# Optimization experiments

Hardware: AMD Instinct MI355X
Metric: run time of the kernel (lower is better)

The kernel has to match this reference:

```python
import jax, jax.numpy as jnp
import numpy as np

ALPHA = 1.702
LIMIT = 7.0
EPS = 1e-5
TOP_K = 4


def setup_inputs() -> dict:
    key = jax.random.key(0)
    ks = jax.random.split(key, 8)
    B, S, H, I, E = 2, 512, 2048, 2048, 16
    return {
        "x": jax.random.normal(ks[0], (B, S, H), jnp.float32),
        "norm_w": jnp.ones((H,), jnp.float32),
        "gate_w": jax.random.normal(ks[1], (E, H), jnp.float32) * 0.02,
        "gate_b": jax.random.normal(ks[2], (E,), jnp.float32) * 0.02,
        "w1": jax.random.normal(ks[3], (E, 2 * I, H), jnp.float32) * 0.02,
        "b1": jax.random.normal(ks[4], (E, 2 * I), jnp.float32) * 0.02,
        "w2": jax.random.normal(ks[5], (E, H, I), jnp.float32) * 0.02,
        "b2": jax.random.normal(ks[6], (E, H), jnp.float32) * 0.02,
    }


def reference(x, norm_w, gate_w, gate_b, w1, b1, w2, b2):
    B, S, H = x.shape
    M = B * S
    E = gate_w.shape[0]
    xf = x.reshape(M, H)
    # RMSNorm
    t = xf * jax.lax.rsqrt(jnp.mean(xf * xf, axis=-1, keepdims=True) + EPS) * norm_w
    # Router: top-k over logits, then softmax over the selected k (sm_first=False)
    logits = t @ gate_w.T + gate_b  # [M, E]
    vals, idx = jax.lax.top_k(logits, TOP_K)
    gates_k = jax.nn.softmax(vals, axis=-1)  # [M, k]
    # Scatter top-k gate weights into dense [M, E] combine matrix
    G = jnp.zeros((M, E), x.dtype).at[jnp.arange(M)[:, None], idx].set(gates_k)
    # Expert MLP1 (all experts, combined sparsely below): [E, M, 2I]
    h = jnp.einsum('mh,eoh->emo', t, w1) + b1[:, None, :]
    # SwiGLU with clamp (gpt-oss): interleaved gate/linear columns
    a = jnp.minimum(h[..., ::2], LIMIT)
    b = jnp.clip(h[..., 1::2], -LIMIT, LIMIT)
    act = a * jax.nn.sigmoid(ALPHA * a) * (b + 1.0)  # [E, M, I]
    # Expert MLP2: [E, M, H]
    y = jnp.einsum('emi,edi->emd', act, w2) + b2[:, None, :]
    # Combine with gate weights (gammas scale full per-expert output incl. bias)
    delta = jnp.einsum('me,emd->md', G, y)
    return x + delta.reshape(B, S, H)
```

## Files before the change

kernel.cpp:

```cpp
#include <hip/hip_runtime.h>
#include <hip/hip_bf16.h>

constexpr int MTOK = 1024;
constexpr int HDIM = 2048;
constexpr int IDIM = 2048;
constexpr int NEXP = 16;
constexpr int TOPK = 4;
constexpr int NA   = MTOK * TOPK;

#define ALPHA_C 1.702f
#define LIMIT_C 7.0f
#define RMS_EPS 1e-5f

using short8 = __attribute__((ext_vector_type(8))) short;
using f32x4  = __attribute__((ext_vector_type(4))) float;

__device__ __forceinline__ unsigned short f2bf(float f) {
    unsigned u = __builtin_bit_cast(unsigned, f);
    u += 0x7fffu + ((u >> 16) & 1u);
    return (unsigned short)(u >> 16);
}

__device__ __forceinline__ unsigned pack2bf(float lo, float hi) {
    return (unsigned)f2bf(lo) | ((unsigned)f2bf(hi) << 16);
}

__device__ __forceinline__ short8 cvt8(const float4 a, const float4 b) {
    union { short8 s; unsigned u[4]; } r;
    r.u[0] = pack2bf(a.x, a.y);
    r.u[1] = pack2bf(a.z, a.w);
    r.u[2] = pack2bf(b.x, b.y);
    r.u[3] = pack2bf(b.z, b.w);
    return r.s;
}

__global__ __launch_bounds__(256) void k_router(
    const float* __restrict__ x, const float* __restrict__ norm_w,
    const float* __restrict__ gate_w, const float* __restrict__ gate_b,
    float* __restrict__ out,
    unsigned short* __restrict__ t_bf,
    int* __restrict__ counts, int* __restrict__ idx_of,
    int* __restrict__ slot_of, float* __restrict__ gate_mk)
{
    __shared__ float t_lds[HDIM];
    __shared__ float red[4];
    __shared__ float logits[NEXP];

    const int m   = blockIdx.x;
    const int tid = threadIdx.x;
    const float* xr = x + (size_t)m * HDIM;

    float4 v0 = ((const float4*)xr)[tid * 2];
    float4 v1 = ((const float4*)xr)[tid * 2 + 1];
    ((float4*)(out + (size_t)m * HDIM))[tid * 2]     = v0;
    ((float4*)(out + (size_t)m * HDIM))[tid * 2 + 1] = v1;

    float ss = v0.x*v0.x + v0.y*v0.y + v0.z*v0.z + v0.w*v0.w
             + v1.x*v1.x + v1.y*v1.y + v1.z*v1.z + v1.w*v1.w;
    #pragma unroll
    for (int off = 32; off > 0; off >>= 1) ss += __shfl_down(ss, off);
    if ((tid & 63) == 0) red[tid >> 6] = ss;
    __syncthreads();
    float tot = red[0] + red[1] + red[2] + red[3];
    float scale = rsqrtf(tot / (float)HDIM + RMS_EPS);

    float4 n0 = ((const float4*)norm_w)[tid * 2];
    float4 n1 = ((const float4*)norm_w)[tid * 2 + 1];
    float t[8];
    t[0]=v0.x*scale*n0.x; t[1]=v0.y*scale*n0.y; t[2]=v0.z*scale*n0.z; t[3]=v0.w*scale*n0.w;
    t[4]=v1.x*scale*n1.x; t[5]=v1.y*scale*n1.y; t[6]=v1.z*scale*n1.z; t[7]=v1.w*scale*n1.w;
    short8 pk;
    #pragma unroll
    for (int j = 0; j < 8; ++j) {
        t_lds[tid * 8 + j] = t[j];
        pk[j] = (short)f2bf(t[j]);
    }
    *(short8*)(t_bf + (size_t)m * HDIM + tid * 8) = pk;
    __syncthreads();

    const int e = tid >> 4, j = tid & 15;
    const float4* gw4 = (const float4*)(gate_w + (size_t)e * HDIM);
    const float4* tl4 = (const float4*)t_lds;
    float part = 0.f;
    for (int h4 = j; h4 < HDIM / 4; h4 += 16) {
        float4 g = gw4[h4], tv = tl4[h4];
        part += g.x*tv.x + g.y*tv.y + g.z*tv.z + g.w*tv.w;
    }
    #pragma unroll
    for (int off = 8; off > 0; off >>= 1) part += __shfl_xor(part, off);
    if (j == 0) logits[e] = part + gate_b[e];
    __syncthreads();

    if (tid == 0) {
        float lv[NEXP];
        #pragma unroll
        for (int q = 0; q < NEXP; ++q) lv[q] = logits[q];
        int   sel[TOPK];
        float sv[TOPK];
        #pragma unroll
        for (int k = 0; k < TOPK; ++k) {
            float best = -1e30f; int bi = 0;
            for (int q = 0; q < NEXP; ++q)
                if (lv[q] > best) { best = lv[q]; bi = q; }
            sel[k] = bi; sv[k] = best; lv[bi] = -1e30f;
        }
        float mx = sv[0], s = 0.f, g[TOPK];
        #pragma unroll
        for (int k = 0; k < TOPK; ++k) { g[k] = __expf(sv[k] - mx); s += g[k]; }
        float inv = 1.f / s;
        #pragma unroll
        for (int k = 0; k < TOPK; ++k) {
            int a = m * TOPK + k;
            int slot = atomicAdd(&counts[sel[k]], 1);
            idx_of[a]  = sel[k];
            slot_of[a] = slot;
            gate_mk[a] = g[k] * inv;
        }
    }
}

__global__ void k_remap(const int* __restrict__ idx_of, const int* __restrict__ slot_of,
                        const float* __restrict__ gate_mk, const int* __restrict__ counts,
                        int* __restrict__ token_of, float* __restrict__ gate_row)
{
    int a = blockIdx.x * blockDim.x + threadIdx.x;
    if (a >= NA) return;
    int e = idx_of[a];
    int off = 0;
    for (int q = 0; q < NEXP; ++q) off += (q < e) ? counts[q] : 0;
    int r = off + slot_of[a];
    token_of[r] = a >> 2;
    gate_row[r] = gate_mk[a];
}

__global__ __launch_bounds__(256) void k_gemm1(
    const unsigned short* __restrict__ t_bf,
    const float* __restrict__ w1, const float* __restrict__ b1,
    const int* __restrict__ counts, const int* __restrict__ token_of,
    unsigned short* __restrict__ act)
{
    __shared__ unsigned char lB[2][5120];

    const int e = blockIdx.z;
    int ne = 0, roff = 0;
    #pragma unroll
    for (int q = 0; q < NEXP; ++q) {
        int cq = counts[q];
        roff += (q < e) ? cq : 0;
        ne    = (q == e) ? cq : ne;
    }
    const int brow = blockIdx.y * 320;
    if (brow >= ne) return;
    const int i0 = blockIdx.x * 32;
    const int tid = threadIdx.x;

    const int wv = tid >> 6, ln = tid & 63;
    const int lr = ln & 15, lk = ln >> 4;
    const int br = tid >> 2, bp = tid & 3;

    const unsigned short* aptr[5];
    #pragma unroll
    for (int mf = 0; mf < 5; ++mf) {
        int rg = brow + wv * 80 + mf * 16 + lr;
        int tok = token_of[roff + (rg < ne ? rg : 0)];
        aptr[mf] = t_bf + (size_t)tok * HDIM + lk * 8;
    }
    const int o = (br < 32) ? (2 * (i0 + br)) : (2 * (i0 + br - 32) + 1);
    const float* bsrc = w1 + ((size_t)e * (2 * IDIM) + o) * HDIM + bp * 8;

    short8 aS[2][5];
    float4 bS[4][2];
    f32x4  acc[5][4] = {};

    {
        float4 p0 = *(const float4*)(bsrc);
        float4 p1 = *(const float4*)(bsrc + 4);
        *(short8*)(&lB[0][br * 80 + bp * 16]) = cvt8(p0, p1);
    }
    bS[1][0] = *(const float4*)(bsrc + 32);  bS[1][1] = *(const float4*)(bsrc + 36);
    bS[2][0] = *(const float4*)(bsrc + 64);  bS[2][1] = *(const float4*)(bsrc + 68);
    bS[3][0] = *(const float4*)(bsrc + 96);  bS[3][1] = *(const float4*)(bsrc + 100);
    #pragma unroll
    for (int mf = 0; mf < 5; ++mf) {
        aS[0][mf] = *(const short8*)(aptr[mf]);
        aS[1][mf] = *(const short8*)(aptr[mf] + 32);
    }
    asm volatile("s_waitcnt lgkmcnt(0)" ::: "memory");
    __builtin_amdgcn_s_barrier();

#define GSTEP(T, P)                                                                          \
    {                                                                                        \
        const int t_ = (T);                                                                  \
        if (t_ + 1 < 64)                                                                     \
            *(short8*)(&lB[((P) & 1) ^ 1][br * 80 + bp * 16]) =                              \
                cvt8(bS[((P) + 1) & 3][0], bS[((P) + 1) & 3][1]);                            \
        if (t_ + 4 < 64) {                                                                   \
            bS[(P)][0] = *(const float4*)(bsrc + (t_ + 4) * 32);                             \
            bS[(P)][1] = *(const float4*)(bsrc + (t_ + 4) * 32 + 4);                         \
        }                                                                                    \
        short8 bfr[4];                                                                       \
        _Pragma("unroll")                                                                    \
        for (int n = 0; n < 4; ++n)                                                          \
            bfr[n] = *(const short8*)(&lB[(P) & 1][(n * 16 + lr) * 80 + lk * 16]);           \
        _Pragma("unroll")                                                                    \
        for (int mf = 0; mf < 5; ++mf)                                                       \
            _Pragma("unroll")                                                                \
            for (int n = 0; n < 4; ++n)                                                      \
                acc[mf][n] = __builtin_amdgcn_mfma_f32_16x16x32_bf16(                        \
                    aS[(P) & 1][mf], bfr[n], acc[mf][n], 0, 0, 0);                           \
        if (t_ + 2 < 64) {                                                                   \
            _Pragma("unroll")                                                                \
            for (int mf = 0; mf < 5; ++mf)                                                   \
                aS[(P) & 1][mf] = *(const short8*)(aptr[mf] + (t_ + 2) * 32);                \
        }                                                                                    \
        asm volatile("s_waitcnt lgkmcnt(0)" ::: "memory");                                   \
        __builtin_amdgcn_s_barrier();                                                        \
    }

    for (int t16 = 0; t16 < 16; ++t16) {
        const int tb = t16 * 4;
        GSTEP(tb + 0, 0)
        GSTEP(tb + 1, 1)
        GSTEP(tb + 2, 2)
        GSTEP(tb + 3, 3)
    }
#undef GSTEP

    #pragma unroll
    for (int n = 0; n < 2; ++n) {
        const int i = i0 + n * 16 + lr;
        const float ba = b1[(size_t)e * (2 * IDIM) + 2 * i];
        const float bb = b1[(size_t)e * (2 * IDIM) + 2 * i + 1];
        #pragma unroll
        for (int mf = 0; mf < 5; ++mf) {
            #pragma unroll
            for (int r = 0; r < 4; ++r) {
                const int rg = brow + wv * 80 + mf * 16 + lk * 4 + r;
                if (rg < ne) {
                    float ha = acc[mf][n][r] + ba;
                    float hb = acc[mf][n + 2][r] + bb;
                    float a = fminf(ha, LIMIT_C);
                    float b = fminf(fmaxf(hb, -LIMIT_C), LIMIT_C);
                    float s = 1.f / (1.f + __expf(-ALPHA_C * a));
                    act[(size_t)(roff + rg) * IDIM + i] = f2bf(a * s * (b + 1.f));
                }
            }
        }
    }
}

__global__ __launch_bounds__(256) void k_gemm2(
    const unsigned short* __restrict__ act,
    const float* __restrict__ w2, const float* __restrict__ b2,
    const int* __restrict__ counts, const int* __restrict__ token_of,
    const float* __restrict__ gate_row,
    float* __restrict__ out)
{
    __shared__ unsigned char lB[2][5120];

    const int e = blockIdx.z;
    int ne = 0, roff = 0;
    #pragma unroll
    for (int q = 0; q < NEXP; ++q) {
        int cq = counts[q];
        roff += (q < e) ? cq : 0;
        ne    = (q == e) ? cq : ne;
    }
    const int brow = blockIdx.y * 320;
    if (brow >= ne) return;
    const int ks = blockIdx.x & 1;
    const int d0 = (blockIdx.x >> 1) * 64;
    const int kbeg = ks * (IDIM / 2);
    const int tid = threadIdx.x;

    const int wv = tid >> 6, ln = tid & 63;
    const int lr = ln & 15, lk = ln >> 4;
    const int br = tid >> 2, bp = tid & 3;

    const unsigned short* aptr[5];
    #pragma unroll
    for (int mf = 0; mf < 5; ++mf) {
        int rg = brow + wv * 80 + mf * 16 + lr;
        int rc = (rg < ne) ? rg : 0;
        aptr[mf] = act + (size_t)(roff + rc) * IDIM + kbeg + lk * 8;
    }
    const float* bsrc = w2 + ((size_t)e * HDIM + d0 + br) * IDIM + kbeg + bp * 8;

    short8 aS[2][5];
    float4 bS[4][2];
    f32x4  acc[5][4] = {};

    {
        float4 p0 = *(const float4*)(bsrc);
        float4 p1 = *(const float4*)(bsrc + 4);
        *(short8*)(&lB[0][br * 80 + bp * 16]) = cvt8(p0, p1);
    }
    bS[1][0] = *(const float4*)(bsrc + 32);  bS[1][1] = *(const float4*)(bsrc + 36);
    bS[2][0] = *(const float4*)(bsrc + 64);  bS[2][1] = *(const float4*)(bsrc + 68);
    bS[3][0] = *(const float4*)(bsrc + 96);  bS[3][1] = *(const float4*)(bsrc + 100);
    #pragma unroll
    for (int mf = 0; mf < 5; ++mf) {
        aS[0][mf] = *(const short8*)(aptr[mf]);
        aS[1][mf] = *(const short8*)(aptr[mf] + 32);
    }
    asm volatile("s_waitcnt lgkmcnt(0)" ::: "memory");
    __builtin_amdgcn_s_barrier();

#define GSTEP(T, P)                                                                          \
    {                                                                                        \
        const int t_ = (T);                                                                  \
        if (t_ + 1 < 32)                                                                     \
            *(short8*)(&lB[((P) & 1) ^ 1][br * 80 + bp * 16]) =                              \
                cvt8(bS[((P) + 1) & 3][0], bS[((P) + 1) & 3][1]);                            \
        if (t_ + 4 < 32) {                                                                   \
            bS[(P)][0] = *(const float4*)(bsrc + (t_ + 4) * 32);                             \
            bS[(P)][1] = *(const float4*)(bsrc + (t_ + 4) * 32 + 4);                         \
        }                                                                                    \
        short8 bfr[4];                                                                       \
        _Pragma("unroll")                                                                    \
        for (int n = 0; n < 4; ++n)                                                          \
            bfr[n] = *(const short8*)(&lB[(P) & 1][(n * 16 + lr) * 80 + lk * 16]);           \
        _Pragma("unroll")                                                                    \
        for (int mf = 0; mf < 5; ++mf)                                                       \
            _Pragma("unroll")                                                                \
            for (int n = 0; n < 4; ++n)                                                      \
                acc[mf][n] = __builtin_amdgcn_mfma_f32_16x16x32_bf16(                        \
                    aS[(P) & 1][mf], bfr[n], acc[mf][n], 0, 0, 0);                           \
        if (t_ + 2 < 32) {                                                                   \
            _Pragma("unroll")                                                                \
            for (int mf = 0; mf < 5; ++mf)                                                   \
                aS[(P) & 1][mf] = *(const short8*)(aptr[mf] + (t_ + 2) * 32);                \
        }                                                                                    \
        asm volatile("s_waitcnt lgkmcnt(0)" ::: "memory");                                   \
        __builtin_amdgcn_s_barrier();                                                        \
    }

    for (int t8 = 0; t8 < 8; ++t8) {
        const int tb = t8 * 4;
        GSTEP(tb + 0, 0)
        GSTEP(tb + 1, 1)
        GSTEP(tb + 2, 2)
        GSTEP(tb + 3, 3)
    }
#undef GSTEP

    #pragma unroll
    for (int mf = 0; mf < 5; ++mf) {
        #pragma unroll
        for (int r = 0; r < 4; ++r) {
            const int rg = brow + wv * 80 + mf * 16 + lk * 4 + r;
            if (rg >= ne) continue;
            const int tok = token_of[roff + rg];
            const float g = gate_row[roff + rg];
            float* orow = out + (size_t)tok * HDIM;
            #pragma unroll
            for (int n = 0; n < 4; ++n) {
                const int d = d0 + n * 16 + lr;
                float v = g * acc[mf][n][r];
                if (ks == 0) v += g * b2[(size_t)e * HDIM + d];
                atomicAdd(orow + d, v);
            }
        }
    }
}

extern "C" void kernel_launch(void* const* d_in, const int* in_sizes, int n_in,
                              void* d_out, int out_size, void* d_ws, size_t ws_size,
                              hipStream_t stream) {
    const float* x      = (const float*)d_in[0];
    const float* norm_w = (const float*)d_in[1];
    const float* gate_w = (const float*)d_in[2];
    const float* gate_b = (const float*)d_in[3];
    const float* w1     = (const float*)d_in[4];
    const float* b1     = (const float*)d_in[5];
    const float* w2     = (const float*)d_in[6];
    const float* b2     = (const float*)d_in[7];
    float* out = (float*)d_out;

    char* ws = (char*)d_ws;
    size_t off = 0;
    unsigned short* t_bf = (unsigned short*)(ws + off); off += (size_t)MTOK * HDIM * 2;
    unsigned short* actb = (unsigned short*)(ws + off); off += (size_t)NA * IDIM * 2;
    int*   counts   = (int*)(ws + off);   off += 256;
    int*   idx_of   = (int*)(ws + off);   off += (size_t)NA * 4;
    int*   slot_of  = (int*)(ws + off);   off += (size_t)NA * 4;
    float* gate_mk  = (float*)(ws + off); off += (size_t)NA * 4;
    int*   token_of = (int*)(ws + off);   off += (size_t)NA * 4;
    float* gate_row = (float*)(ws + off); off += (size_t)NA * 4;

    (void)hipMemsetAsync(counts, 0, 256, stream);
    k_router<<<MTOK, 256, 0, stream>>>(x, norm_w, gate_w, gate_b, out, t_bf,
                                       counts, idx_of, slot_of, gate_mk);
    k_remap<<<NA / 256, 256, 0, stream>>>(idx_of, slot_of, gate_mk, counts,
                                          token_of, gate_row);
    k_gemm1<<<dim3(IDIM / 32, (MTOK + 319) / 320, NEXP), 256, 0, stream>>>(
        t_bf, w1, b1, counts, token_of, actb);
    k_gemm2<<<dim3((HDIM / 64) * 2, (MTOK + 319) / 320, NEXP), 256, 0, stream>>>(
        actb, w2, b2, counts, token_of, gate_row, out);
}
```

Measured before the change: 481.2 us.

## Replace gemm2 atomic scatter with bf16 staging plus combine kernel; widen K-step

The second expert GEMM no longer splits K in two or scatter-adds gated results into the output with float atomics. It now writes per-assignment bf16 rows with bias into a staging buffer, and a new combine kernel gathers the top-k rows per token, applies the gate weights and adds the residual. Both GEMMs also process a 64-wide K slice per barrier step, with two LDS sub-tiles and a deeper register prefetch ring, which halves the number of barriers. This removes atomic traffic and barrier overhead. In exchange it adds a launch, an extra bf16 round-trip of the expert outputs through memory, and lower precision in the combined sum.

```diff
diff --git a/kernel.cpp b/kernel.cpp
--- a/kernel.cpp
+++ b/kernel.cpp
@@ -37,7 +37,6 @@
 __global__ __launch_bounds__(256) void k_router(
     const float* __restrict__ x, const float* __restrict__ norm_w,
     const float* __restrict__ gate_w, const float* __restrict__ gate_b,
-    float* __restrict__ out,
     unsigned short* __restrict__ t_bf,
     int* __restrict__ counts, int* __restrict__ idx_of,
     int* __restrict__ slot_of, float* __restrict__ gate_mk)
@@ -52,9 +51,6 @@
 
     float4 v0 = ((const float4*)xr)[tid * 2];
     float4 v1 = ((const float4*)xr)[tid * 2 + 1];
-    ((float4*)(out + (size_t)m * HDIM))[tid * 2]     = v0;
-    ((float4*)(out + (size_t)m * HDIM))[tid * 2 + 1] = v1;
-
     float ss = v0.x*v0.x + v0.y*v0.y + v0.z*v0.z + v0.w*v0.w
              + v1.x*v1.x + v1.y*v1.y + v1.z*v1.z + v1.w*v1.w;
     #pragma unroll
@@ -120,8 +116,8 @@
 }
 
 __global__ void k_remap(const int* __restrict__ idx_of, const int* __restrict__ slot_of,
-                        const float* __restrict__ gate_mk, const int* __restrict__ counts,
-                        int* __restrict__ token_of, float* __restrict__ gate_row)
+                        const int* __restrict__ counts,
+                        int* __restrict__ token_of, int* __restrict__ rowidx)
 {
     int a = blockIdx.x * blockDim.x + threadIdx.x;
     if (a >= NA) return;
@@ -130,7 +126,7 @@
     for (int q = 0; q < NEXP; ++q) off += (q < e) ? counts[q] : 0;
     int r = off + slot_of[a];
     token_of[r] = a >> 2;
-    gate_row[r] = gate_mk[a];
+    rowidx[a]   = r;
 }
 
 __global__ __launch_bounds__(256) void k_gemm1(
@@ -139,7 +135,7 @@
     const int* __restrict__ counts, const int* __restrict__ token_of,
     unsigned short* __restrict__ act)
 {
-    __shared__ unsigned char lB[2][5120];
+    __shared__ unsigned char lB[2][2][5120];
 
     const int e = blockIdx.z;
     int ne = 0, roff = 0;
@@ -166,63 +162,87 @@
         aptr[mf] = t_bf + (size_t)tok * HDIM + lk * 8;
     }
     const int o = (br < 32) ? (2 * (i0 + br)) : (2 * (i0 + br - 32) + 1);
-    const float* bsrc = w1 + ((size_t)e * (2 * IDIM) + o) * HDIM + bp * 8;
-
-    short8 aS[2][5];
-    float4 bS[4][2];
+    const float* bsrc = w1 + ((size_t)e * (2 * IDIM) + o) * HDIM + bp * 16;
+
+    float4 bS0[4], bS1[4], bS2[4], bS3[4];
+    short8 aA0[5], aA1[5];
     f32x4  acc[5][4] = {};
+
+    constexpr int NT = 32;
 
     {
         float4 p0 = *(const float4*)(bsrc);
         float4 p1 = *(const float4*)(bsrc + 4);
-        *(short8*)(&lB[0][br * 80 + bp * 16]) = cvt8(p0, p1);
-    }
-    bS[1][0] = *(const float4*)(bsrc + 32);  bS[1][1] = *(const float4*)(bsrc + 36);
-    bS[2][0] = *(const float4*)(bsrc + 64);  bS[2][1] = *(const float4*)(bsrc + 68);
-    bS[3][0] = *(const float4*)(bsrc + 96);  bS[3][1] = *(const float4*)(bsrc + 100);
+        float4 p2 = *(const float4*)(bsrc + 8);
+        float4 p3 = *(const float4*)(bsrc + 12);
+        *(short8*)(&lB[0][bp >> 1][br * 80 + (bp & 1) * 32])      = cvt8(p0, p1);
+        *(short8*)(&lB[0][bp >> 1][br * 80 + (bp & 1) * 32 + 16]) = cvt8(p2, p3);
+    }
+    #pragma unroll
+    for (int j = 0; j < 4; ++j) {
+        bS1[j] = *(const float4*)(bsrc + 64  + j * 4);
+        bS2[j] = *(const float4*)(bsrc + 128 + j * 4);
+        bS3[j] = *(const float4*)(bsrc + 192 + j * 4);
+    }
     #pragma unroll
     for (int mf = 0; mf < 5; ++mf) {
-        aS[0][mf] = *(const short8*)(aptr[mf]);
-        aS[1][mf] = *(const short8*)(aptr[mf] + 32);
+        aA0[mf] = *(const short8*)(aptr[mf]);
+        aA1[mf] = *(const short8*)(aptr[mf] + 32);
     }
     asm volatile("s_waitcnt lgkmcnt(0)" ::: "memory");
     __builtin_amdgcn_s_barrier();
 
-#define GSTEP(T, P)                                                                          \
-    {                                                                                        \
-        const int t_ = (T);                                                                  \
-        if (t_ + 1 < 64)                                                                     \
-            *(short8*)(&lB[((P) & 1) ^ 1][br * 80 + bp * 16]) =                              \
-                cvt8(bS[((P) + 1) & 3][0], bS[((P) + 1) & 3][1]);                            \
-        if (t_ + 4 < 64) {                                                                   \
-            bS[(P)][0] = *(const float4*)(bsrc + (t_ + 4) * 32);                             \
-            bS[(P)][1] = *(const float4*)(bsrc + (t_ + 4) * 32 + 4);                         \
-        }                                                                                    \
-        short8 bfr[4];                                                                       \
-        _Pragma("unroll")                                                                    \
-        for (int n = 0; n < 4; ++n)                                                          \
-            bfr[n] = *(const short8*)(&lB[(P) & 1][(n * 16 + lr) * 80 + lk * 16]);           \
-        _Pragma("unroll")                                                                    \
-        for (int mf = 0; mf < 5; ++mf)                                                       \
-            _Pragma("unroll")                                                                \
-            for (int n = 0; n < 4; ++n)                                                      \
-                acc[mf][n] = __builtin_amdgcn_mfma_f32_16x16x32_bf16(                        \
-                    aS[(P) & 1][mf], bfr[n], acc[mf][n], 0, 0, 0);                           \
-        if (t_ + 2 < 64) {                                                                   \
-            _Pragma("unroll")                                                                \
-            for (int mf = 0; mf < 5; ++mf)                                                   \
-                aS[(P) & 1][mf] = *(const short8*)(aptr[mf] + (t_ + 2) * 32);                \
-        }                                                                                    \
-        asm volatile("s_waitcnt lgkmcnt(0)" ::: "memory");                                   \
-        __builtin_amdgcn_s_barrier();                                                        \
-    }
-
-    for (int t16 = 0; t16 < 16; ++t16) {
-        const int tb = t16 * 4;
-        GSTEP(tb + 0, 0)
-        GSTEP(tb + 1, 1)
-        GSTEP(tb + 2, 2)
-        GSTEP(tb + 3, 3)
+#define GSTEP(T_, SPUB, SISS)                                                            \
+    {                                                                                    \
+        const int t_ = (T_);                                                             \
+        const int c_ = t_ & 1;                                                           \
+        if (t_ + 1 < NT) {                                         \
+            *(short8*)(&lB[c_ ^ 1][bp >> 1][br * 80 + (bp & 1) * 32])      =             \
+                cvt8(SPUB[0], SPUB[1]);                                                  \
+            *(short8*)(&lB[c_ ^ 1][bp >> 1][br * 80 + (bp & 1) * 32 + 16]) =             \
+                cvt8(SPUB[2], SPUB[3]);                                                  \
+        }                                                                                \
+        if (t_ + 3 < NT) {                                           \
+            _Pragma("unroll")                                                            \
+            for (int j = 0; j < 4; ++j)                                                  \
+                SISS[j] = *(const float4*)(bsrc + (t_ + 3) * 64 + j * 4);                \
+        }                                                                                \
+        short8 bfr[4];                                                                   \
+        _Pragma("unroll")                                                                \
+        for (int n = 0; n < 4; ++n)                                                      \
+            bfr[n] = *(const short8*)(&lB[c_][0][(n * 16 + lr) * 80 + lk * 16]);         \
+        _Pragma("unroll")                                                                \
+        for (int mf = 0; mf < 5; ++mf)                                                   \
+            _Pragma("unroll")                                                            \
+            for (int n = 0; n < 4; ++n)                                                  \
+                acc[mf][n] = __builtin_amdgcn_mfma_f32_16x16x32_bf16(                    \
+                    aA0[mf], bfr[n], acc[mf][n], 0, 0, 0);                               \
+        _Pragma("unroll")                                                                \
+        for (int n = 0; n < 4; ++n)                                                      \
+            bfr[n] = *(const short8*)(&lB[c_][1][(n * 16 + lr) * 80 + lk * 16]);         \
+        _Pragma("unroll")                                                                \
+        for (int mf = 0; mf < 5; ++mf)                                                   \
+            _Pragma("unroll")                                                            \
+            for (int n = 0; n < 4; ++n)                                                  \
+                acc[mf][n] = __builtin_amdgcn_mfma_f32_16x16x32_bf16(                    \
+                    aA1[mf], bfr[n], acc[mf][n], 0, 0, 0);                               \
+        if (t_ + 1 < NT) {                           \
+            _Pragma("unroll")                                                            \
+            for (int mf = 0; mf < 5; ++mf) {                                             \
+                aA0[mf] = *(const short8*)(aptr[mf] + (t_ + 1) * 64);                    \
+                aA1[mf] = *(const short8*)(aptr[mf] + (t_ + 1) * 64 + 32);               \
+            }                                                                            \
+        }                                                                                \
+        asm volatile("s_waitcnt lgkmcnt(0)" ::: "memory");                               \
+        __builtin_amdgcn_s_barrier();                                                    \
+    }
+
+    for (int t8 = 0; t8 < NT / 4; ++t8) {
+        const int tb = t8 * 4;
+        GSTEP(tb + 0, bS1, bS3)
+        GSTEP(tb + 1, bS2, bS0)
+        GSTEP(tb + 2, bS3, bS1)
+        GSTEP(tb + 3, bS0, bS2)
     }
 #undef GSTEP
 
@@ -253,10 +273,9 @@
     const unsigned short* __restrict__ act,
     const float* __restrict__ w2, const float* __restrict__ b2,
     const int* __restrict__ counts, const int* __restrict__ token_of,
-    const float* __restrict__ gate_row,
-    float* __restrict__ out)
+    unsigned short* __restrict__ ybuf)
 {
-    __shared__ unsigned char lB[2][5120];
+    __shared__ unsigned char lB[2][2][5120];
 
     const int e = blockIdx.z;
     int ne = 0, roff = 0;
@@ -268,9 +287,7 @@
     }
     const int brow = blockIdx.y * 320;
     if (brow >= ne) return;
-    const int ks = blockIdx.x & 1;
-    const int d0 = (blockIdx.x >> 1) * 64;
-    const int kbeg = ks * (IDIM / 2);
+    const int d0 = blockIdx.x * 64;
     const int tid = threadIdx.x;
 
     const int wv = tid >> 6, ln = tid & 63;
@@ -282,65 +299,89 @@
     for (int mf = 0; mf < 5; ++mf) {
         int rg = brow + wv * 80 + mf * 16 + lr;
         int rc = (rg < ne) ? rg : 0;
-        aptr[mf] = act + (size_t)(roff + rc) * IDIM + kbeg + lk * 8;
-    }
-    const float* bsrc = w2 + ((size_t)e * HDIM + d0 + br) * IDIM + kbeg + bp * 8;
-
-    short8 aS[2][5];
-    float4 bS[4][2];
+        aptr[mf] = act + (size_t)(roff + rc) * IDIM + lk * 8;
+    }
+    const float* bsrc = w2 + ((size_t)e * HDIM + d0 + br) * IDIM + bp * 16;
+
+    float4 bS0[4], bS1[4], bS2[4], bS3[4];
+    short8 aA0[5], aA1[5];
     f32x4  acc[5][4] = {};
+
+    constexpr int NT = 32;
 
     {
         float4 p0 = *(const float4*)(bsrc);
         float4 p1 = *(const float4*)(bsrc + 4);
-        *(short8*)(&lB[0][br * 80 + bp * 16]) = cvt8(p0, p1);
-    }
-    bS[1][0] = *(const float4*)(bsrc + 32);  bS[1][1] = *(const float4*)(bsrc + 36);
-    bS[2][0] = *(const float4*)(bsrc + 64);  bS[2][1] = *(const float4*)(bsrc + 68);
-    bS[3][0] = *(const float4*)(bsrc + 96);  bS[3][1] = *(const float4*)(bsrc + 100);
+        float4 p2 = *(const float4*)(bsrc + 8);
+        float4 p3 = *(const float4*)(bsrc + 12);
+        *(short8*)(&lB[0][bp >> 1][br * 80 + (bp & 1) * 32])      = cvt8(p0, p1);
+        *(short8*)(&lB[0][bp >> 1][br * 80 + (bp & 1) * 32 + 16]) = cvt8(p2, p3);
+    }
+    #pragma unroll
+    for (int j = 0; j < 4; ++j) {
+        bS1[j] = *(const float4*)(bsrc + 64  + j * 4);
+        bS2[j] = *(const float4*)(bsrc + 128 + j * 4);
+        bS3[j] = *(const float4*)(bsrc + 192 + j * 4);
+    }
     #pragma unroll
     for (int mf = 0; mf < 5; ++mf) {
-        aS[0][mf] = *(const short8*)(aptr[mf]);
-        aS[1][mf] = *(const short8*)(aptr[mf] + 32);
+        aA0[mf] = *(const short8*)(aptr[mf]);
+        aA1[mf] = *(const short8*)(aptr[mf] + 32);
     }
     asm volatile("s_waitcnt lgkmcnt(0)" ::: "memory");
     __builtin_amdgcn_s_barrier();
 
-#define GSTEP(T, P)                                                                          \
-    {                                                                                        \
-        const int t_ = (T);                                                                  \
-        if (t_ + 1 < 32)                                                                     \
-            *(short8*)(&lB[((P) & 1) ^ 1][br * 80 + bp * 16]) =                              \
-                cvt8(bS[((P) + 1) & 3][0], bS[((P) + 1) & 3][1]);                            \
-        if (t_ + 4 < 32) {                                                                   \
-            bS[(P)][0] = *(const float4*)(bsrc + (t_ + 4) * 32);                             \
-            bS[(P)][1] = *(const float4*)(bsrc + (t_ + 4) * 32 + 4);                         \
-        }                                                                                    \
-        short8 bfr[4];                                                                       \
-        _Pragma("unroll")                                                                    \
-        for (int n = 0; n < 4; ++n)                                                          \
-            bfr[n] = *(const short8*)(&lB[(P) & 1][(n * 16 + lr) * 80 + lk * 16]);           \
-        _Pragma("unroll")                                                                    \
-        for (int mf = 0; mf < 5; ++mf)                                                       \
-            _Pragma("unroll")                                                                \
-            for (int n = 0; n < 4; ++n)                                                      \
-                acc[mf][n] = __builtin_amdgcn_mfma_f32_16x16x32_bf16(                        \
-                    aS[(P) & 1][mf], bfr[n], acc[mf][n], 0, 0, 0);                           \
-        if (t_ + 2 < 32) {                                                                   \
-            _Pragma("unroll")                                                                \
-            for (int mf = 0; mf < 5; ++mf)                                                   \
-                aS[(P) & 1][mf] = *(const short8*)(aptr[mf] + (t_ + 2) * 32);                \
-        }                                                                                    \
-        asm volatile("s_waitcnt lgkmcnt(0)" ::: "memory");                                   \
-        __builtin_amdgcn_s_barrier();                                                        \
-    }
-
-    for (int t8 = 0; t8 < 8; ++t8) {
+#define GSTEP(T_, SPUB, SISS)                                                            \
+    {                                                                                    \
+        const int t_ = (T_);                                                             \
+        const int c_ = t_ & 1;                                                           \
+        if (t_ + 1 < NT) {                                                               \
+            *(short8*)(&lB[c_ ^ 1][bp >> 1][br * 80 + (bp & 1) * 32])      =             \
+                cvt8(SPUB[0], SPUB[1]);                                                  \
+            *(short8*)(&lB[c_ ^ 1][bp >> 1][br * 80 + (bp & 1) * 32 + 16]) =             \
+                cvt8(SPUB[2], SPUB[3]);                                                  \
+        }                                                                                \
+        if (t_ + 3 < NT) {                                                               \
+            _Pragma("unroll")                                                            \
+            for (int j = 0; j < 4; ++j)                                                  \
+                SISS[j] = *(const float4*)(bsrc + (t_ + 3) * 64 + j * 4);                \
+        }                                                                                \
+        short8 bfr[4];                                                                   \
+        _Pragma("unroll")                                                                \
+        for (int n = 0; n < 4; ++n)                                                      \
+            bfr[n] = *(const short8*)(&lB[c_][0][(n * 16 + lr) * 80 + lk * 16]);         \
+        _Pragma("unroll")                                                                \
+        for (int mf = 0; mf < 5; ++mf)                                                   \
+            _Pragma("unroll")                                                            \
+            for (int n = 0; n < 4; ++n)                                                  \
+                acc[mf][n] = __builtin_amdgcn_mfma_f32_16x16x32_bf16(                    \
+                    aA0[mf], bfr[n], acc[mf][n], 0, 0, 0);                               \
+        _Pragma("unroll")                                                                \
+        for (int n = 0; n < 4; ++n)                                                      \
+            bfr[n] = *(const short8*)(&lB[c_][1][(n * 16 + lr) * 80 + lk * 16]);         \
+        _Pragma("unroll")                                                                \
+        for (int mf = 0; mf < 5; ++mf)                                                   \
+            _Pragma("unroll")                                                            \
+            for (int n = 0; n < 4; ++n)                                                  \
+                acc[mf][n] = __builtin_amdgcn_mfma_f32_16x16x32_bf16(                    \
+                    aA1[mf], bfr[n], acc[mf][n], 0, 0, 0);                               \
+        if (t_ + 1 < NT) {                                                               \
+            _Pragma("unroll")                                                            \
+            for (int mf = 0; mf < 5; ++mf) {                                             \
+                aA0[mf] = *(const short8*)(aptr[mf] + (t_ + 1) * 64);                    \
+                aA1[mf] = *(const short8*)(aptr[mf] + (t_ + 1) * 64 + 32);               \
+            }                                                                            \
+        }                                                                                \
+        asm volatile("s_waitcnt lgkmcnt(0)" ::: "memory");                               \
+        __builtin_amdgcn_s_barrier();                                                    \
+    }
+
+    for (int t8 = 0; t8 < NT / 4; ++t8) {
         const int tb = t8 * 4;
-        GSTEP(tb + 0, 0)
-        GSTEP(tb + 1, 1)
-        GSTEP(tb + 2, 2)
-        GSTEP(tb + 3, 3)
+        GSTEP(tb + 0, bS1, bS3)
+        GSTEP(tb + 1, bS2, bS0)
+        GSTEP(tb + 2, bS3, bS1)
+        GSTEP(tb + 3, bS0, bS2)
     }
 #undef GSTEP
 
@@ -350,18 +391,48 @@
         for (int r = 0; r < 4; ++r) {
             const int rg = brow + wv * 80 + mf * 16 + lk * 4 + r;
             if (rg >= ne) continue;
-            const int tok = token_of[roff + rg];
-            const float g = gate_row[roff + rg];
-            float* orow = out + (size_t)tok * HDIM;
+            unsigned short* yrow = ybuf + (size_t)(roff + rg) * HDIM;
             #pragma unroll
             for (int n = 0; n < 4; ++n) {
                 const int d = d0 + n * 16 + lr;
-                float v = g * acc[mf][n][r];
-                if (ks == 0) v += g * b2[(size_t)e * HDIM + d];
-                atomicAdd(orow + d, v);
+                yrow[d] = f2bf(acc[mf][n][r] + b2[(size_t)e * HDIM + d]);
             }
         }
     }
+}
+
+__global__ __launch_bounds__(256) void k_comb(
+    const float* __restrict__ x, const unsigned short* __restrict__ ybuf,
+    const int* __restrict__ rowidx, const float* __restrict__ gate_mk,
+    float* __restrict__ out)
+{
+    __shared__ int   rws[TOPK];
+    __shared__ float gws[TOPK];
+    const int m = blockIdx.x;
+    const int tid = threadIdx.x;
+    if (tid < TOPK) {
+        rws[tid] = rowidx[m * TOPK + tid];
+        gws[tid] = gate_mk[m * TOPK + tid];
+    }
+    __syncthreads();
+    const int d = tid * 8;
+    float4 o0 = ((const float4*)(x + (size_t)m * HDIM + d))[0];
+    float4 o1 = ((const float4*)(x + (size_t)m * HDIM + d))[1];
+    #pragma unroll
+    for (int k = 0; k < TOPK; ++k) {
+        const float g = gws[k];
+        short8 y = *(const short8*)(ybuf + (size_t)rws[k] * HDIM + d);
+        float yv[8];
+        #pragma unroll
+        for (int j = 0; j < 8; ++j) {
+            unsigned u = ((unsigned)(unsigned short)y[j]) << 16;
+            yv[j] = __builtin_bit_cast(float, u);
+        }
+        o0.x += g * yv[0]; o0.y += g * yv[1]; o0.z += g * yv[2]; o0.w += g * yv[3];
+        o1.x += g * yv[4]; o1.y += g * yv[5]; o1.z += g * yv[6]; o1.w += g * yv[7];
+    }
+    ((float4*)(out + (size_t)m * HDIM + d))[0] = o0;
+    ((float4*)(out + (size_t)m * HDIM + d))[1] = o1;
 }
 
 extern "C" void kernel_launch(void* const* d_in, const int* in_sizes, int n_in,
@@ -381,20 +452,22 @@
     size_t off = 0;
     unsigned short* t_bf = (unsigned short*)(ws + off); off += (size_t)MTOK * HDIM * 2;
     unsigned short* actb = (unsigned short*)(ws + off); off += (size_t)NA * IDIM * 2;
+    unsigned short* ybuf = (unsigned short*)(ws + off); off += (size_t)NA * HDIM * 2;
     int*   counts   = (int*)(ws + off);   off += 256;
     int*   idx_of   = (int*)(ws + off);   off += (size_t)NA * 4;
     int*   slot_of  = (int*)(ws + off);   off += (size_t)NA * 4;
     float* gate_mk  = (float*)(ws + off); off += (size_t)NA * 4;
     int*   token_of = (int*)(ws + off);   off += (size_t)NA * 4;
-    float* gate_row = (float*)(ws + off); off += (size_t)NA * 4;
+    int*   rowidx   = (int*)(ws + off);   off += (size_t)NA * 4;
 
     (void)hipMemsetAsync(counts, 0, 256, stream);
-    k_router<<<MTOK, 256, 0, stream>>>(x, norm_w, gate_w, gate_b, out, t_bf,
+    k_router<<<MTOK, 256, 0, stream>>>(x, norm_w, gate_w, gate_b, t_bf,
                                        counts, idx_of, slot_of, gate_mk);
-    k_remap<<<NA / 256, 256, 0, stream>>>(idx_of, slot_of, gate_mk, counts,
-                                          token_of, gate_row);
+    k_remap<<<NA / 256, 256, 0, stream>>>(idx_of, slot_of, counts,
+                                          token_of, rowidx);
     k_gemm1<<<dim3(IDIM / 32, (MTOK + 319) / 320, NEXP), 256, 0, stream>>>(
         t_bf, w1, b1, counts, token_of, actb);
-    k_gemm2<<<dim3((HDIM / 64) * 2, (MTOK + 319) / 320, NEXP), 256, 0, stream>>>(
-        actb, w2, b2, counts, token_of, gate_row, out);
-}
+    k_gemm2<<<dim3(HDIM / 64, (MTOK + 319) / 320, NEXP), 256, 0, stream>>>(
+        actb, w2, b2, counts, token_of, ybuf);
+    k_comb<<<MTOK, 256, 0, stream>>>(x, ybuf, rowidx, gate_mk, out);
+}
```

Result: faster. 428.4 us (-11.0%).
